# Kernel tuning notes

Hardware: AMD Instinct MI355X
Metric: run time of the kernel (lower is better)

The kernel has to match this reference:

```python
import jax, jax.numpy as jnp
import numpy as np

SCALE = 1.0  # Scaler(scale=1.0) is a fixed multiplicative scale


def setup_inputs() -> dict:
    key = jax.random.key(0)
    ks = jax.random.split(key, 7)
    d = 2048          # in_features == out_features (per-head proj dim)
    out_total = 3 * d # fused QKV weight rows
    r = 8             # LoRA rank
    B, S = 4, 2048
    return {
        "x": jax.random.normal(ks[0], (B, S, d), dtype=jnp.float32),
        "W": jax.random.normal(ks[1], (out_total, d), dtype=jnp.float32) * 0.02,
        "b": jax.random.normal(ks[2], (out_total,), dtype=jnp.float32) * 0.02,
        "A1": jax.random.normal(ks[3], (r, d), dtype=jnp.float32) * 0.02,
        "B1": jax.random.normal(ks[4], (d, r), dtype=jnp.float32) * 0.02,
        "A2": jax.random.normal(ks[5], (r, d), dtype=jnp.float32) * 0.02,
        "B2": jax.random.normal(ks[6], (d, r), dtype=jnp.float32) * 0.02,
    }


def reference(x, W, b, A1, B1, A2, B2):
    # Low-rank deltas for K and V rows: each [out_features, in_features]
    dK = SCALE * (B1 @ A1)            # [d, d]
    dV = SCALE * (B2 @ A2)            # [d, d]
    delta = jnp.concatenate([dK, dV], axis=0)          # [2d, d]
    # zero-pad on top to match full fused weight (Q rows untouched)
    pad_rows = W.shape[0] - delta.shape[0]
    delta_full = jnp.concatenate(
        [jnp.zeros((pad_rows, W.shape[1]), dtype=W.dtype), delta], axis=0
    )                                                    # [3d, d]
    weight = W + delta_full
    # F.linear: x @ weight.T + b
    return jnp.einsum("bsd,od->bso", x, weight) + b
```

## Files before the change

### kernel.cpp

```cpp
#include <hip/hip_runtime.h>
#include <hip/hip_bf16.h>
#include <stdint.h>
#include <stddef.h>

typedef __attribute__((ext_vector_type(8))) __bf16 bf16x8;
typedef __attribute__((ext_vector_type(4))) float  f32x4;
typedef __attribute__((ext_vector_type(8))) unsigned short ushort8;

typedef const void __attribute__((address_space(1)))* as1_cvp;
typedef void       __attribute__((address_space(3)))* as3_vp;

__device__ __forceinline__ void gload_lds16(const void* g, void* l) {
    __builtin_amdgcn_global_load_lds((as1_cvp)g, (as3_vp)l, 16, 0, 0);
}

__device__ __forceinline__ unsigned short f2bf(float f) {
    union { float f; unsigned u; } v; v.f = f;
    unsigned r = v.u + 0x7fffu + ((v.u >> 16) & 1u);
    return (unsigned short)(r >> 16);
}

__global__ __launch_bounds__(256) void cast_x_kernel(
    const float* __restrict__ src, unsigned short* __restrict__ dst, int n8)
{
    int i = blockIdx.x * 256 + threadIdx.x;
    if (i >= n8) return;
    const float4* s = (const float4*)src + (size_t)i * 2;
    float4 a = s[0], c = s[1];
    ushort8 o;
    o[0] = f2bf(a.x); o[1] = f2bf(a.y); o[2] = f2bf(a.z); o[3] = f2bf(a.w);
    o[4] = f2bf(c.x); o[5] = f2bf(c.y); o[6] = f2bf(c.z); o[7] = f2bf(c.w);
    ((ushort8*)dst)[i] = o;
}

__global__ __launch_bounds__(256) void prep_w_kernel(
    const float* __restrict__ W,
    const float* __restrict__ A1, const float* __restrict__ B1,
    const float* __restrict__ A2, const float* __restrict__ B2,
    unsigned short* __restrict__ Wb, int d)
{
    int o  = blockIdx.x;
    int k0 = threadIdx.x * 8;
    const float4* wrow = (const float4*)(W + (size_t)o * d + k0);
    float4 w0 = wrow[0], w1 = wrow[1];
    float acc[8] = {w0.x, w0.y, w0.z, w0.w, w1.x, w1.y, w1.z, w1.w};
    if (o >= d) {
        const float* A  = (o < 2 * d) ? A1 : A2;
        const float* Bm = (o < 2 * d) ? B1 : B2;
        int r0 = o - ((o < 2 * d) ? d : 2 * d);
#pragma unroll
        for (int r = 0; r < 8; ++r) {
            float bb = Bm[(size_t)r0 * 8 + r];
            const float4* arow = (const float4*)(A + (size_t)r * d + k0);
            float4 a0 = arow[0], a1 = arow[1];
            acc[0] += bb * a0.x; acc[1] += bb * a0.y;
            acc[2] += bb * a0.z; acc[3] += bb * a0.w;
            acc[4] += bb * a1.x; acc[5] += bb * a1.y;
            acc[6] += bb * a1.z; acc[7] += bb * a1.w;
        }
    }
    ushort8 ov;
#pragma unroll
    for (int c = 0; c < 8; ++c) ov[c] = f2bf(acc[c]);
    ((ushort8*)(Wb + (size_t)o * d))[threadIdx.x] = ov;
}

constexpr int BM = 128, BN = 128, BK = 32;

__global__ __launch_bounds__(256) void gemm_bt_kernel(
    const unsigned short* __restrict__ Xb,
    const unsigned short* __restrict__ Wb,
    const float* __restrict__ bias,
    float* __restrict__ out,
    int M, int N, int K)
{
    __shared__ __align__(16) unsigned short As[BM * BK];
    __shared__ __align__(16) unsigned short Bs[BN * BK];

    const int tid  = threadIdx.x;
    const int wave = tid >> 6;
    const int lane = tid & 63;
    const int quad = lane >> 4;
    const int lr   = lane & 15;

    const int bm = blockIdx.y * BM;
    const int bn = blockIdx.x * BN;

    const unsigned short* gA[2];
    const unsigned short* gB[2];
    unsigned short* ldsA[2];
    unsigned short* ldsB[2];
#pragma unroll
    for (int t = 0; t < 2; ++t) {
        int L = t * 256 + wave * 64 + lane;
        int m = L >> 2;
        int p = L & 3;
        int c = p ^ ((m >> 1) & 3);
        gA[t] = Xb + (size_t)(bm + m) * K + c * 8;
        gB[t] = Wb + (size_t)(bn + m) * K + c * 8;
        ldsA[t] = &As[(t * 256 + wave * 64) * 8];
        ldsB[t] = &Bs[(t * 256 + wave * 64) * 8];
    }

    const int wm = (wave & 1) * 64;
    const int wn = (wave >> 1) * 64;

    int offA[4], offB[4];
#pragma unroll
    for (int i = 0; i < 4; ++i) {
        int m = wm + i * 16 + lr;
        offA[i] = (m * 4 + (quad ^ ((m >> 1) & 3))) * 8;
        int n = wn + i * 16 + lr;
        offB[i] = (n * 4 + (quad ^ ((n >> 1) & 3))) * 8;
    }

    f32x4 acc[4][4];
#pragma unroll
    for (int i = 0; i < 4; ++i)
#pragma unroll
        for (int j = 0; j < 4; ++j)
            acc[i][j] = (f32x4){0.f, 0.f, 0.f, 0.f};

    for (int kt = 0; kt < K; kt += BK) {
        gload_lds16(gA[0], ldsA[0]);
        gload_lds16(gA[1], ldsA[1]);
        gload_lds16(gB[0], ldsB[0]);
        gload_lds16(gB[1], ldsB[1]);
        gA[0] += BK; gA[1] += BK; gB[0] += BK; gB[1] += BK;
        __syncthreads();

        bf16x8 af[4], bf[4];
#pragma unroll
        for (int i = 0; i < 4; ++i) af[i] = *(const bf16x8*)&As[offA[i]];
#pragma unroll
        for (int j = 0; j < 4; ++j) bf[j] = *(const bf16x8*)&Bs[offB[j]];
#pragma unroll
        for (int i = 0; i < 4; ++i)
#pragma unroll
            for (int j = 0; j < 4; ++j)
                acc[i][j] = __builtin_amdgcn_mfma_f32_16x16x32_bf16(
                    af[i], bf[j], acc[i][j], 0, 0, 0);
        __syncthreads();
    }

#pragma unroll
    for (int j = 0; j < 4; ++j) {
        int col = bn + wn + j * 16 + lr;
        float bv = bias[col];
#pragma unroll
        for (int i = 0; i < 4; ++i) {
            int row = bm + wm + i * 16 + quad * 4;
            float* op = out + (size_t)row * N + col;
#pragma unroll
            for (int r = 0; r < 4; ++r)
                op[(size_t)r * N] = acc[i][j][r] + bv;
        }
    }
}

extern "C" void kernel_launch(void* const* d_in, const int* in_sizes, int n_in,
                              void* d_out, int out_size, void* d_ws, size_t ws_size,
                              hipStream_t stream) {
    const float* x  = (const float*)d_in[0];
    const float* W  = (const float*)d_in[1];
    const float* b  = (const float*)d_in[2];
    const float* A1 = (const float*)d_in[3];
    const float* B1 = (const float*)d_in[4];
    const float* A2 = (const float*)d_in[5];
    const float* B2 = (const float*)d_in[6];
    float* out = (float*)d_out;

    const int d = 2048;
    const int K = d;
    const int N = 3 * d;
    const int M = in_sizes[0] / d;

    unsigned short* Xbf = (unsigned short*)d_ws;
    unsigned short* Wbf = Xbf + (size_t)M * K;

    int n8 = (M * K) / 8;
    cast_x_kernel<<<(n8 + 255) / 256, 256, 0, stream>>>(x, Xbf, n8);

    prep_w_kernel<<<N, 256, 0, stream>>>(W, A1, B1, A2, B2, Wbf, d);

    dim3 grid(N / BN, M / BM);
    gemm_bt_kernel<<<grid, 256, 0, stream>>>(Xbf, Wbf, b, out, M, N, K);
}
```

Before: 534.1 us.

## Use 32x32x16 MFMA with BK=64 tiles and merge prep kernels

Switches the GEMM inner loop from 16x16x32 MFMA tiles to 32x32x16 MFMA, doubles the K tile to 64 with an 8-way XOR swizzle in LDS, and reorganises the global-to-LDS loads to match. It also fuses the x cast and the weight prep into one launch. The goal is fewer LDS reads per FLOP, half as many barriers per K, and one less launch. LDS use doubles, which can lower occupancy, and the epilogue store pattern changes.

```diff
diff --git a/kernel.cpp b/kernel.cpp
--- a/kernel.cpp
+++ b/kernel.cpp
@@ -3,9 +3,9 @@
 #include <stdint.h>
 #include <stddef.h>
 
-typedef __attribute__((ext_vector_type(8))) __bf16 bf16x8;
-typedef __attribute__((ext_vector_type(4))) float  f32x4;
-typedef __attribute__((ext_vector_type(8))) unsigned short ushort8;
+typedef __attribute__((ext_vector_type(8)))  __bf16 bf16x8;
+typedef __attribute__((ext_vector_type(16))) float  f32x16;
+typedef __attribute__((ext_vector_type(8)))  unsigned short ushort8;
 
 typedef const void __attribute__((address_space(1)))* as1_cvp;
 typedef void       __attribute__((address_space(3)))* as3_vp;
@@ -20,52 +20,53 @@
     return (unsigned short)(r >> 16);
 }
 
-__global__ __launch_bounds__(256) void cast_x_kernel(
-    const float* __restrict__ src, unsigned short* __restrict__ dst, int n8)
-{
-    int i = blockIdx.x * 256 + threadIdx.x;
-    if (i >= n8) return;
-    const float4* s = (const float4*)src + (size_t)i * 2;
-    float4 a = s[0], c = s[1];
-    ushort8 o;
-    o[0] = f2bf(a.x); o[1] = f2bf(a.y); o[2] = f2bf(a.z); o[3] = f2bf(a.w);
-    o[4] = f2bf(c.x); o[5] = f2bf(c.y); o[6] = f2bf(c.z); o[7] = f2bf(c.w);
-    ((ushort8*)dst)[i] = o;
-}
-
-__global__ __launch_bounds__(256) void prep_w_kernel(
+__global__ __launch_bounds__(256) void prep_kernel(
+    const float* __restrict__ x,
     const float* __restrict__ W,
     const float* __restrict__ A1, const float* __restrict__ B1,
     const float* __restrict__ A2, const float* __restrict__ B2,
-    unsigned short* __restrict__ Wb, int d)
+    unsigned short* __restrict__ Xb, unsigned short* __restrict__ Wb,
+    int d, int nW, int n8)
 {
-    int o  = blockIdx.x;
-    int k0 = threadIdx.x * 8;
-    const float4* wrow = (const float4*)(W + (size_t)o * d + k0);
-    float4 w0 = wrow[0], w1 = wrow[1];
-    float acc[8] = {w0.x, w0.y, w0.z, w0.w, w1.x, w1.y, w1.z, w1.w};
-    if (o >= d) {
-        const float* A  = (o < 2 * d) ? A1 : A2;
-        const float* Bm = (o < 2 * d) ? B1 : B2;
-        int r0 = o - ((o < 2 * d) ? d : 2 * d);
+    int blk = blockIdx.x;
+    if (blk < nW) {
+        int o  = blk;
+        int k0 = threadIdx.x * 8;
+        const float4* wrow = (const float4*)(W + (size_t)o * d + k0);
+        float4 w0 = wrow[0], w1 = wrow[1];
+        float acc[8] = {w0.x, w0.y, w0.z, w0.w, w1.x, w1.y, w1.z, w1.w};
+        if (o >= d) {
+            const float* A  = (o < 2 * d) ? A1 : A2;
+            const float* Bm = (o < 2 * d) ? B1 : B2;
+            int r0 = o - ((o < 2 * d) ? d : 2 * d);
 #pragma unroll
-        for (int r = 0; r < 8; ++r) {
-            float bb = Bm[(size_t)r0 * 8 + r];
-            const float4* arow = (const float4*)(A + (size_t)r * d + k0);
-            float4 a0 = arow[0], a1 = arow[1];
-            acc[0] += bb * a0.x; acc[1] += bb * a0.y;
-            acc[2] += bb * a0.z; acc[3] += bb * a0.w;
-            acc[4] += bb * a1.x; acc[5] += bb * a1.y;
-            acc[6] += bb * a1.z; acc[7] += bb * a1.w;
+            for (int r = 0; r < 8; ++r) {
+                float bb = Bm[(size_t)r0 * 8 + r];
+                const float4* arow = (const float4*)(A + (size_t)r * d + k0);
+                float4 a0 = arow[0], a1 = arow[1];
+                acc[0] += bb * a0.x; acc[1] += bb * a0.y;
+                acc[2] += bb * a0.z; acc[3] += bb * a0.w;
+                acc[4] += bb * a1.x; acc[5] += bb * a1.y;
+                acc[6] += bb * a1.z; acc[7] += bb * a1.w;
+            }
         }
+        ushort8 ov;
+#pragma unroll
+        for (int c = 0; c < 8; ++c) ov[c] = f2bf(acc[c]);
+        ((ushort8*)(Wb + (size_t)o * d))[threadIdx.x] = ov;
+    } else {
+        int i = (blk - nW) * 256 + threadIdx.x;
+        if (i >= n8) return;
+        const float4* s = (const float4*)x + (size_t)i * 2;
+        float4 a = s[0], c = s[1];
+        ushort8 o;
+        o[0] = f2bf(a.x); o[1] = f2bf(a.y); o[2] = f2bf(a.z); o[3] = f2bf(a.w);
+        o[4] = f2bf(c.x); o[5] = f2bf(c.y); o[6] = f2bf(c.z); o[7] = f2bf(c.w);
+        ((ushort8*)Xb)[i] = o;
     }
-    ushort8 ov;
-#pragma unroll
-    for (int c = 0; c < 8; ++c) ov[c] = f2bf(acc[c]);
-    ((ushort8*)(Wb + (size_t)o * d))[threadIdx.x] = ov;
 }
 
-constexpr int BM = 128, BN = 128, BK = 32;
+constexpr int BM = 128, BN = 128, BK = 64;
 
 __global__ __launch_bounds__(256) void gemm_bt_kernel(
     const unsigned short* __restrict__ Xb,
@@ -80,80 +81,74 @@
     const int tid  = threadIdx.x;
     const int wave = tid >> 6;
     const int lane = tid & 63;
-    const int quad = lane >> 4;
-    const int lr   = lane & 15;
+    const int half = lane >> 5;
+    const int ln32 = lane & 31;
 
     const int bm = blockIdx.y * BM;
     const int bn = blockIdx.x * BN;
 
-    const unsigned short* gA[2];
-    const unsigned short* gB[2];
-    unsigned short* ldsA[2];
-    unsigned short* ldsB[2];
-#pragma unroll
-    for (int t = 0; t < 2; ++t) {
-        int L = t * 256 + wave * 64 + lane;
-        int m = L >> 2;
-        int p = L & 3;
-        int c = p ^ ((m >> 1) & 3);
-        gA[t] = Xb + (size_t)(bm + m) * K + c * 8;
-        gB[t] = Wb + (size_t)(bn + m) * K + c * 8;
-        ldsA[t] = &As[(t * 256 + wave * 64) * 8];
-        ldsB[t] = &Bs[(t * 256 + wave * 64) * 8];
-    }
+    const int m0 = tid >> 3;
+    const int c0 = (tid & 7) ^ (m0 & 7);
+    const size_t goff = (size_t)m0 * K + c0 * 8;
 
     const int wm = (wave & 1) * 64;
     const int wn = (wave >> 1) * 64;
 
-    int offA[4], offB[4];
+    const int r7 = ln32 & 7;
+    int dofs[4];
 #pragma unroll
-    for (int i = 0; i < 4; ++i) {
-        int m = wm + i * 16 + lr;
-        offA[i] = (m * 4 + (quad ^ ((m >> 1) & 3))) * 8;
-        int n = wn + i * 16 + lr;
-        offB[i] = (n * 4 + (quad ^ ((n >> 1) & 3))) * 8;
+    for (int s = 0; s < 4; ++s) dofs[s] = ((s * 2 + half) ^ r7) * 8;
+    int baseA[2], baseB[2];
+#pragma unroll
+    for (int i = 0; i < 2; ++i) {
+        baseA[i] = (wm + i * 32 + ln32) * 64;
+        baseB[i] = (wn + i * 32 + ln32) * 64;
     }
 
-    f32x4 acc[4][4];
+    f32x16 acc[2][2];
 #pragma unroll
-    for (int i = 0; i < 4; ++i)
+    for (int i = 0; i < 2; ++i)
 #pragma unroll
-        for (int j = 0; j < 4; ++j)
-            acc[i][j] = (f32x4){0.f, 0.f, 0.f, 0.f};
+        for (int j = 0; j < 2; ++j)
+#pragma unroll
+            for (int r = 0; r < 16; ++r) acc[i][j][r] = 0.f;
 
     for (int kt = 0; kt < K; kt += BK) {
-        gload_lds16(gA[0], ldsA[0]);
-        gload_lds16(gA[1], ldsA[1]);
-        gload_lds16(gB[0], ldsB[0]);
-        gload_lds16(gB[1], ldsB[1]);
-        gA[0] += BK; gA[1] += BK; gB[0] += BK; gB[1] += BK;
+        const unsigned short* pa = Xb + (size_t)bm * K + kt + goff;
+        const unsigned short* pb = Wb + (size_t)bn * K + kt + goff;
+#pragma unroll
+        for (int t = 0; t < 4; ++t) {
+            gload_lds16(pa + (size_t)t * 32 * K, &As[(t * 256 + wave * 64) * 8]);
+            gload_lds16(pb + (size_t)t * 32 * K, &Bs[(t * 256 + wave * 64) * 8]);
+        }
         __syncthreads();
 
-        bf16x8 af[4], bf[4];
 #pragma unroll
-        for (int i = 0; i < 4; ++i) af[i] = *(const bf16x8*)&As[offA[i]];
-#pragma unroll
-        for (int j = 0; j < 4; ++j) bf[j] = *(const bf16x8*)&Bs[offB[j]];
-#pragma unroll
-        for (int i = 0; i < 4; ++i)
-#pragma unroll
-            for (int j = 0; j < 4; ++j)
-                acc[i][j] = __builtin_amdgcn_mfma_f32_16x16x32_bf16(
-                    af[i], bf[j], acc[i][j], 0, 0, 0);
+        for (int s = 0; s < 4; ++s) {
+            bf16x8 a0 = *(const bf16x8*)&As[baseA[0] + dofs[s]];
+            bf16x8 a1 = *(const bf16x8*)&As[baseA[1] + dofs[s]];
+            bf16x8 b0 = *(const bf16x8*)&Bs[baseB[0] + dofs[s]];
+            bf16x8 b1 = *(const bf16x8*)&Bs[baseB[1] + dofs[s]];
+            acc[0][0] = __builtin_amdgcn_mfma_f32_32x32x16_bf16(a0, b0, acc[0][0], 0, 0, 0);
+            acc[0][1] = __builtin_amdgcn_mfma_f32_32x32x16_bf16(a0, b1, acc[0][1], 0, 0, 0);
+            acc[1][0] = __builtin_amdgcn_mfma_f32_32x32x16_bf16(a1, b0, acc[1][0], 0, 0, 0);
+            acc[1][1] = __builtin_amdgcn_mfma_f32_32x32x16_bf16(a1, b1, acc[1][1], 0, 0, 0);
+        }
         __syncthreads();
     }
 
 #pragma unroll
-    for (int j = 0; j < 4; ++j) {
-        int col = bn + wn + j * 16 + lr;
+    for (int j = 0; j < 2; ++j) {
+        int col = bn + wn + j * 32 + ln32;
         float bv = bias[col];
 #pragma unroll
-        for (int i = 0; i < 4; ++i) {
-            int row = bm + wm + i * 16 + quad * 4;
-            float* op = out + (size_t)row * N + col;
+        for (int i = 0; i < 2; ++i) {
+            int rbase = bm + wm + i * 32 + 4 * half;
 #pragma unroll
-            for (int r = 0; r < 4; ++r)
-                op[(size_t)r * N] = acc[i][j][r] + bv;
+            for (int reg = 0; reg < 16; ++reg) {
+                int row = rbase + (reg & 3) + 8 * (reg >> 2);
+                out[(size_t)row * N + col] = acc[i][j][reg] + bv;
+            }
         }
     }
 }
@@ -179,9 +174,9 @@
     unsigned short* Wbf = Xbf + (size_t)M * K;
 
     int n8 = (M * K) / 8;
-    cast_x_kernel<<<(n8 + 255) / 256, 256, 0, stream>>>(x, Xbf, n8);
-
-    prep_w_kernel<<<N, 256, 0, stream>>>(W, A1, B1, A2, B2, Wbf, d);
+    int castBlocks = (n8 + 255) / 256;
+    prep_kernel<<<N + castBlocks, 256, 0, stream>>>(x, W, A1, B1, A2, B2,
+                                                    Xbf, Wbf, d, N, n8);
 
     dim3 grid(N / BN, M / BM);
     gemm_bt_kernel<<<grid, 256, 0, stream>>>(Xbf, Wbf, b, out, M, N, K);
```

Result: faster. 505.2 us (-5.4%).
